# Kernel tuning notes

Measured on AMD Instinct MI355X. Metric: run time of the kernel, lower is better.

Reference implementation:

```python
import jax, jax.numpy as jnp
import numpy as np

HIDDEN = 2048
HEADS = 16
HEAD_DIM = HIDDEN // HEADS  # 128
ROPE_BASE = 10000.0


def _rope_cos_sin(seq_len, head_dim, dtype):
    inv_freq = 1.0 / (ROPE_BASE ** (jnp.arange(0, head_dim, 2, dtype=jnp.float32) / head_dim))
    pos = jnp.arange(seq_len, dtype=jnp.float32)
    freqs = pos[:, None] * inv_freq[None, :]            # [S, D/2]
    emb = jnp.concatenate([freqs, freqs], axis=-1)      # [S, D]
    return jnp.cos(emb).astype(dtype), jnp.sin(emb).astype(dtype)


def _rotate_half(x):
    x1, x2 = jnp.split(x, 2, axis=-1)
    return jnp.concatenate([-x2, x1], axis=-1)


def apply_rope(q, k, seq_len):
    # q, k: [B, H, S, Dh]
    cos, sin = _rope_cos_sin(seq_len, q.shape[-1], q.dtype)
    q = q * cos + _rotate_half(q) * sin
    k = k * cos + _rotate_half(k) * sin
    return q, k


def setup_inputs() -> dict:
    key = jax.random.key(0)
    ks = jax.random.split(key, 5)
    B, S = 2, 2048
    scale = 1.0 / np.sqrt(HIDDEN)
    return {
        "hidden_states": jax.random.normal(ks[0], (B, S, HIDDEN), dtype=jnp.float32),
        "w_qkv": jax.random.normal(ks[1], (3 * HIDDEN, HIDDEN), dtype=jnp.float32) * scale,
        "b_qkv": jnp.zeros((3 * HIDDEN,), dtype=jnp.float32),
        "w_dense": jax.random.normal(ks[2], (HIDDEN, HIDDEN), dtype=jnp.float32) * scale,
        "b_dense": jnp.zeros((HIDDEN,), dtype=jnp.float32),
    }


def reference(hidden_states, w_qkv, b_qkv, w_dense, b_dense):
    B, S, _ = hidden_states.shape
    qkv = hidden_states @ w_qkv.T + b_qkv                      # [B, S, 3*H*Dh]
    qkv = qkv.reshape(B, S, 3, HEADS, HEAD_DIM)
    qkv = jnp.transpose(qkv, (2, 0, 3, 1, 4))                  # [3, B, H, S, Dh]
    q, k, v = qkv[0], qkv[1], qkv[2]

    # pos_encoding.apply_to_qk -> RoPE
    q, k = apply_rope(q, k, S)

    scale = HEAD_DIM ** (-0.5)
    scores = jnp.einsum("bhqd,bhkd->bhqk", q, k) * scale       # [B, H, S, S]

    # pos_encoding.apply_to_scores -> causal additive mask
    causal = jnp.tril(jnp.ones((S, S), dtype=bool))
    scores = jnp.where(causal, scores, jnp.finfo(scores.dtype).min)

    attn = jax.nn.softmax(scores, axis=-1)
    out = jnp.einsum("bhqk,bhkd->bhqd", attn, v)               # [B, H, S, Dh]
    out = jnp.transpose(out, (0, 2, 1, 3)).reshape(B, S, HIDDEN)
    return out @ w_dense.T + b_dense
```

## Files before the change

kernel.cpp:

```cpp
#include <hip/hip_runtime.h>
#include <hip/hip_bf16.h>
#include <stdint.h>

#define HID 2048
#define NHEAD 16
#define DHEAD 128
#define BB 2
#define SS 2048
#define MM (BB*SS)
#define NQKV (3*HID)
#define NT (SS/64)

typedef __attribute__((ext_vector_type(8))) short bf16x8;
typedef __attribute__((ext_vector_type(4))) float f32x4;
typedef unsigned short ushort_t;

__device__ __forceinline__ f32x4 mfma16(bf16x8 a, bf16x8 b, f32x4 c) {
    return __builtin_amdgcn_mfma_f32_16x16x32_bf16(a, b, c, 0, 0, 0);
}

__device__ __forceinline__ float bf2f(ushort_t u) {
    unsigned int x = ((unsigned int)u) << 16;
    return __builtin_bit_cast(float, x);
}
__device__ __forceinline__ ushort_t f2bf(float f) {
    unsigned int x = __builtin_bit_cast(unsigned int, f);
    unsigned int r = (x + 0x7FFFu + ((x >> 16) & 1u)) >> 16;
    return (ushort_t)r;
}

__device__ __forceinline__ void cvt8(const float* __restrict__ g, ushort_t* l) {
    float4 a = *(const float4*)g;
    float4 b = *(const float4*)(g + 4);
    union { ushort_t u[8]; uint4 v; } t;
    t.u[0] = f2bf(a.x); t.u[1] = f2bf(a.y); t.u[2] = f2bf(a.z); t.u[3] = f2bf(a.w);
    t.u[4] = f2bf(b.x); t.u[5] = f2bf(b.y); t.u[6] = f2bf(b.z); t.u[7] = f2bf(b.w);
    *(uint4*)l = t.v;
}

__device__ __forceinline__ void gload16(const ushort_t* g, ushort_t* l) {
    __builtin_amdgcn_global_load_lds(
        (const __attribute__((address_space(1))) unsigned int*)(const void*)g,
        (__attribute__((address_space(3))) unsigned int*)(void*)l,
        16, 0, 0);
}

__global__ void cvt3_kernel(const float* __restrict__ a, ushort_t* __restrict__ da, int na,
                            const float* __restrict__ b, ushort_t* __restrict__ db, int nb,
                            const float* __restrict__ c, ushort_t* __restrict__ dc, int nc)
{
    int i = blockIdx.x * blockDim.x + threadIdx.x;
    if (i < na) {
        cvt8(a + (size_t)i * 8, da + (size_t)i * 8);
    } else if (i < na + nb) {
        int j = i - na;
        cvt8(b + (size_t)j * 8, db + (size_t)j * 8);
    } else if (i < na + nb + nc) {
        int j = i - na - nb;
        cvt8(c + (size_t)j * 8, dc + (size_t)j * 8);
    }
}

#define BM 256
#define BN 128
#define BKK 64
#define NTK (HID/BKK)
#define ASZ (BM*BKK)
#define BSZ (BN*BKK)
#define BUFSZ (ASZ+BSZ)

__global__ __launch_bounds__(512, 1) void qkv_gemm_fast(
    const ushort_t* __restrict__ X,
    const ushort_t* __restrict__ W,
    const float* __restrict__ bias,
    ushort_t* __restrict__ qws,
    ushort_t* __restrict__ kws,
    ushort_t* __restrict__ vtws)
{
    __shared__ __align__(16) ushort_t smem[3 * BUFSZ];

    const int tid  = threadIdx.x;
    const int lane = tid & 63;
    const int w    = tid >> 6;
    const int wm   = w >> 1;
    const int wn   = w & 1;
    const int quad = lane >> 4;
    const int l15  = lane & 15;
    const int sub  = (lane & 7) ^ (lane >> 3);
    const int rloc = lane >> 3;
    const int m0 = blockIdx.y * BM;
    const int n0 = blockIdx.x * BN;
    const bool vmode = (n0 >= 2 * HID);

    const ushort_t* gA = X + (size_t)m0 * HID;
    const ushort_t* gB = W + (size_t)n0 * HID;

    f32x4 acc[4][4];
#pragma unroll
    for (int i = 0; i < 4; i++)
#pragma unroll
        for (int j = 0; j < 4; j++)
#pragma unroll
            for (int e = 0; e < 4; e++) acc[i][j][e] = 0.f;

    auto STAGE = [&](int bufi, int t) {
        ushort_t* lA = smem + bufi * BUFSZ;
        ushort_t* lB = lA + ASZ;
        const ushort_t* ga = gA + t * BKK;
        const ushort_t* gb = gB + t * BKK;
#pragma unroll
        for (int i = 0; i < 4; i++) {
            int blk = w * 4 + i;
            gload16(ga + (size_t)(blk * 8 + rloc) * HID + sub * 8, lA + blk * 512);
        }
#pragma unroll
        for (int i = 0; i < 2; i++) {
            int blk = w * 2 + i;
            gload16(gb + (size_t)(blk * 8 + rloc) * HID + sub * 8, lB + blk * 512);
        }
    };

    auto COMPUTE = [&](int bufi) {
        const ushort_t* lA = smem + bufi * BUFSZ;
        const ushort_t* lB = lA + ASZ;
        bf16x8 af[2][4], bfr[2][4];
#pragma unroll
        for (int kk = 0; kk < 2; kk++) {
            const int cs = ((kk * 4 + quad) ^ (l15 & 7)) << 3;
#pragma unroll
            for (int mb = 0; mb < 4; mb++)
                af[kk][mb] = *(const bf16x8*)(lA + (wm * 64 + mb * 16 + l15) * 64 + cs);
#pragma unroll
            for (int nb = 0; nb < 4; nb++)
                bfr[kk][nb] = *(const bf16x8*)(lB + (wn * 64 + nb * 16 + l15) * 64 + cs);
        }
        __builtin_amdgcn_s_setprio(1);
        if (!vmode) {
#pragma unroll
            for (int kk = 0; kk < 2; kk++)
#pragma unroll
                for (int mb = 0; mb < 4; mb++)
#pragma unroll
                    for (int nb = 0; nb < 4; nb++)
                        acc[mb][nb] = mfma16(af[kk][mb], bfr[kk][nb], acc[mb][nb]);
        } else {
#pragma unroll
            for (int kk = 0; kk < 2; kk++)
#pragma unroll
                for (int mb = 0; mb < 4; mb++)
#pragma unroll
                    for (int nb = 0; nb < 4; nb++)
                        acc[mb][nb] = mfma16(bfr[kk][nb], af[kk][mb], acc[mb][nb]);
        }
        __builtin_amdgcn_s_setprio(0);
    };

    STAGE(0, 0);
    STAGE(1, 1);
    asm volatile("s_waitcnt vmcnt(6)" ::: "memory");
    __builtin_amdgcn_s_barrier();

    int buf = 0;
    for (int t = 0; t < NTK - 2; t++) {
        int b2 = buf + 2; if (b2 >= 3) b2 -= 3;
        STAGE(b2, t + 2);
        COMPUTE(buf);
        asm volatile("s_waitcnt vmcnt(6)" ::: "memory");
        __builtin_amdgcn_s_barrier();
        buf++; if (buf == 3) buf = 0;
    }
    COMPUTE(buf);
    asm volatile("s_waitcnt vmcnt(0)" ::: "memory");
    __builtin_amdgcn_s_barrier();
    buf++; if (buf == 3) buf = 0;
    COMPUTE(buf);

    if (!vmode) {
#pragma unroll
        for (int nb = 0; nb < 4; nb++) {
            int n = n0 + wn * 64 + nb * 16 + l15;
            float bv = bias[n];
            int mat = n >> 11;
            int h   = (n >> 7) & 15;
            int d   = n & 127;
            ushort_t* dst = (mat == 0) ? qws : kws;
#pragma unroll
            for (int mb = 0; mb < 4; mb++) {
#pragma unroll
                for (int r = 0; r < 4; r++) {
                    int m = m0 + wm * 64 + mb * 16 + quad * 4 + r;
                    int b = m >> 11;
                    int s = m & 2047;
                    dst[(((size_t)(b * 16 + h) * SS) + s) * DHEAD + d] =
                        f2bf(acc[mb][nb][r] + bv);
                }
            }
        }
    } else {
        const int b = m0 >> 11;
#pragma unroll
        for (int nb = 0; nb < 4; nb++) {
#pragma unroll
            for (int r = 0; r < 4; r++) {
                int n = n0 + wn * 64 + nb * 16 + quad * 4 + r;
                float bv = bias[n];
                int h = (n >> 7) & 15;
                int d = n & 127;
#pragma unroll
                for (int mb = 0; mb < 4; mb++) {
                    int s = (m0 & 2047) + wm * 64 + mb * 16 + l15;
                    vtws[(((size_t)(b * 16 + h) * DHEAD) + d) * SS + s] =
                        f2bf(acc[mb][nb][r] + bv);
                }
            }
        }
    }
}

__global__ __launch_bounds__(512, 1) void dense_gemm_fast(
    const ushort_t* __restrict__ A,
    const ushort_t* __restrict__ W,
    const float* __restrict__ bias,
    float* __restrict__ out)
{
    __shared__ __align__(16) ushort_t smem[3 * BUFSZ];

    const int tid  = threadIdx.x;
    const int lane = tid & 63;
    const int w    = tid >> 6;
    const int wm   = w >> 1;
    const int wn   = w & 1;
    const int quad = lane >> 4;
    const int l15  = lane & 15;
    const int sub  = (lane & 7) ^ (lane >> 3);
    const int rloc = lane >> 3;
    const int m0 = blockIdx.y * BM;
    const int n0 = blockIdx.x * BN;

    const ushort_t* gA = A + (size_t)m0 * HID;
    const ushort_t* gB = W + (size_t)n0 * HID;

    f32x4 acc[4][4];
#pragma unroll
    for (int i = 0; i < 4; i++)
#pragma unroll
        for (int j = 0; j < 4; j++)
#pragma unroll
            for (int e = 0; e < 4; e++) acc[i][j][e] = 0.f;

    auto STAGE = [&](int bufi, int t) {
        ushort_t* lA = smem + bufi * BUFSZ;
        ushort_t* lB = lA + ASZ;
        const ushort_t* ga = gA + t * BKK;
        const ushort_t* gb = gB + t * BKK;
#pragma unroll
        for (int i = 0; i < 4; i++) {
            int blk = w * 4 + i;
            gload16(ga + (size_t)(blk * 8 + rloc) * HID + sub * 8, lA + blk * 512);
        }
#pragma unroll
        for (int i = 0; i < 2; i++) {
            int blk = w * 2 + i;
            gload16(gb + (size_t)(blk * 8 + rloc) * HID + sub * 8, lB + blk * 512);
        }
    };

    auto COMPUTE = [&](int bufi) {
        const ushort_t* lA = smem + bufi * BUFSZ;
        const ushort_t* lB = lA + ASZ;
        bf16x8 af[2][4], bfr[2][4];
#pragma unroll
        for (int kk = 0; kk < 2; kk++) {
            const int cs = ((kk * 4 + quad) ^ (l15 & 7)) << 3;
#pragma unroll
            for (int mb = 0; mb < 4; mb++)
                af[kk][mb] = *(const bf16x8*)(lA + (wm * 64 + mb * 16 + l15) * 64 + cs);
#pragma unroll
            for (int nb = 0; nb < 4; nb++)
                bfr[kk][nb] = *(const bf16x8*)(lB + (wn * 64 + nb * 16 + l15) * 64 + cs);
        }
        __builtin_amdgcn_s_setprio(1);
#pragma unroll
        for (int kk = 0; kk < 2; kk++)
#pragma unroll
            for (int mb = 0; mb < 4; mb++)
#pragma unroll
                for (int nb = 0; nb < 4; nb++)
                    acc[mb][nb] = mfma16(af[kk][mb], bfr[kk][nb], acc[mb][nb]);
        __builtin_amdgcn_s_setprio(0);
    };

    STAGE(0, 0);
    STAGE(1, 1);
    asm volatile("s_waitcnt vmcnt(6)" ::: "memory");
    __builtin_amdgcn_s_barrier();

    int buf = 0;
    for (int t = 0; t < NTK - 2; t++) {
        int b2 = buf + 2; if (b2 >= 3) b2 -= 3;
        STAGE(b2, t + 2);
        COMPUTE(buf);
        asm volatile("s_waitcnt vmcnt(6)" ::: "memory");
        __builtin_amdgcn_s_barrier();
        buf++; if (buf == 3) buf = 0;
    }
    COMPUTE(buf);
    asm volatile("s_waitcnt vmcnt(0)" ::: "memory");
    __builtin_amdgcn_s_barrier();
    buf++; if (buf == 3) buf = 0;
    COMPUTE(buf);

#pragma unroll
    for (int nb = 0; nb < 4; nb++) {
        int n = n0 + wn * 64 + nb * 16 + l15;
        float bv = bias[n];
#pragma unroll
        for (int mb = 0; mb < 4; mb++) {
#pragma unroll
            for (int r = 0; r < 4; r++) {
                int m = m0 + wm * 64 + mb * 16 + quad * 4 + r;
                out[(size_t)m * HID + n] = acc[mb][nb][r] + bv;
            }
        }
    }
}

__global__ void rope_kernel2(ushort_t* __restrict__ qws, ushort_t* __restrict__ kws)
{
    int idx = blockIdx.x * blockDim.x + threadIdx.x;
    int d2 = idx & 63;
    int s  = idx >> 6;

    float inv_freq = exp2f(-(float)d2 * (13.287712379549449f / 64.f));
    float fr = (float)s * inv_freq;
    float sn, cs;
    sincosf(fr, &sn, &cs);

    size_t base0 = (size_t)s * DHEAD + d2;
#pragma unroll
    for (int bh = 0; bh < BB * NHEAD; bh++) {
        size_t base = base0 + (size_t)bh * (SS * DHEAD);
        float q1 = bf2f(qws[base]);
        float q2 = bf2f(qws[base + 64]);
        qws[base]      = f2bf(q1 * cs - q2 * sn);
        qws[base + 64] = f2bf(q2 * cs + q1 * sn);
        float k1 = bf2f(kws[base]);
        float k2 = bf2f(kws[base + 64]);
        kws[base]      = f2bf(k1 * cs - k2 * sn);
        kws[base + 64] = f2bf(k2 * cs + k1 * sn);
    }
}

#define LDP 72

__global__ __launch_bounds__(256, 2) void attn_kernel4(
    const ushort_t* __restrict__ qws,
    const ushort_t* __restrict__ kws,
    const ushort_t* __restrict__ vtws,
    ushort_t* __restrict__ aout)
{
    __shared__ __align__(16) ushort_t k_s[64 * 128];
    __shared__ __align__(16) ushort_t vt_s[128 * 64];
    __shared__ __align__(16) ushort_t pA_s[4][16 * LDP];
    __shared__ __align__(16) ushort_t pB_s[4][16 * LDP];

    const int tid  = threadIdx.x;
    const int lane = tid & 63;
    const int w    = tid >> 6;
    const int quad = lane >> 4;
    const int l15  = lane & 15;

    const int g  = blockIdx.x;
    const int bh = (g & 7) | (((g >> 3) & 3) << 3);
    const int tA = g >> 5;
    const int tB = NT - 1 - tA;
    const int qA = tA * 64, qB = tB * 64;
    const size_t qk_base = (size_t)bh * SS * DHEAD;

    bf16x8 qa[4], qb[4];
    {
        const ushort_t* rowA = qws + qk_base + (size_t)(qA + w * 16 + l15) * DHEAD;
        const ushort_t* rowB = qws + qk_base + (size_t)(qB + w * 16 + l15) * DHEAD;
#pragma unroll
        for (int kc = 0; kc < 4; kc++) {
            qa[kc] = *(const bf16x8*)(rowA + kc * 32 + quad * 8);
            qb[kc] = *(const bf16x8*)(rowB + kc * 32 + quad * 8);
        }
    }

    bf16x8 ones;
#pragma unroll
    for (int i = 0; i < 8; i++) ones[i] = (short)0x3F80;

    f32x4 oA[8], oB[8], lA, lB;
#pragma unroll
    for (int i = 0; i < 8; i++)
#pragma unroll
        for (int e = 0; e < 4; e++) { oA[i][e] = 0.f; oB[i][e] = 0.f; }
#pragma unroll
    for (int e = 0; e < 4; e++) { lA[e] = 0.f; lB[e] = 0.f; }

    const int srowK = lane >> 4;
    const int srowV = lane >> 3;
    const int ccgV  = (lane & 7) ^ (lane >> 3);

    const int q_baseA = qA + w * 16 + quad * 4;
    const int q_baseB = qB + w * 16 + quad * 4;
    const int xorv = l15 & 7;

    const float scale2 = 0.12753102015727466f;
    const float FM = 16.0f;

    for (int j = 0; j <= tB; j++) {
        const int kb = j * 64;
        __syncthreads();
#pragma unroll
        for (int i = 0; i < 4; i++) {
            int P = i * 4 + w;
            int row = P * 4 + srowK;
            int ccg = l15 ^ (((P & 1) * 4) + srowK);
            gload16(kws + qk_base + (size_t)(kb + row) * DHEAD + ccg * 8,
                    k_s + P * 512);
        }
#pragma unroll
        for (int i = 0; i < 4; i++) {
            int P = i * 4 + w;
            int row = P * 8 + srowV;
            gload16(vtws + qk_base + (size_t)row * SS + kb + ccgV * 8,
                    vt_s + P * 512);
        }
        __syncthreads();

        f32x4 sA[4], sB[4];
#pragma unroll
        for (int nb = 0; nb < 4; nb++)
#pragma unroll
            for (int e = 0; e < 4; e++) { sA[nb][e] = 0.f; sB[nb][e] = 0.f; }

        if (j <= tA) {
#pragma unroll
            for (int kc = 0; kc < 4; kc++) {
#pragma unroll
                for (int nb = 0; nb < 4; nb++) {
                    int cc_s = (kc * 4 + quad) ^ xorv;
                    bf16x8 kf = *(const bf16x8*)(k_s + (nb * 16 + l15) * 128 + cc_s * 8);
                    sA[nb] = mfma16(qa[kc], kf, sA[nb]);
                    sB[nb] = mfma16(qb[kc], kf, sB[nb]);
                }
            }
#pragma unroll
            for (int nb = 0; nb < 4; nb++) {
                int kidx = kb + nb * 16 + l15;
#pragma unroll
                for (int r = 0; r < 4; r++) {
                    float pa = exp2f(sA[nb][r] * scale2 - FM);
                    float pb = exp2f(sB[nb][r] * scale2 - FM);
                    pa = (kidx <= q_baseA + r) ? pa : 0.f;
                    pb = (kidx <= q_baseB + r) ? pb : 0.f;
                    pA_s[w][(quad * 4 + r) * LDP + nb * 16 + l15] = f2bf(pa);
                    pB_s[w][(quad * 4 + r) * LDP + nb * 16 + l15] = f2bf(pb);
                }
            }
#pragma unroll
            for (int kc = 0; kc < 2; kc++) {
                bf16x8 pa = *(const bf16x8*)(pA_s[w] + l15 * LDP + kc * 32 + quad * 8);
                bf16x8 pb = *(const bf16x8*)(pB_s[w] + l15 * LDP + kc * 32 + quad * 8);
                lA = mfma16(pa, ones, lA);
                lB = mfma16(pb, ones, lB);
#pragma unroll
                for (int db = 0; db < 8; db++) {
                    int cc_s = (kc * 4 + quad) ^ xorv;
                    bf16x8 vf = *(const bf16x8*)(vt_s + (db * 16 + l15) * 64 + cc_s * 8);
                    oA[db] = mfma16(pa, vf, oA[db]);
                    oB[db] = mfma16(pb, vf, oB[db]);
                }
            }
        } else {
#pragma unroll
            for (int kc = 0; kc < 4; kc++) {
#pragma unroll
                for (int nb = 0; nb < 4; nb++) {
                    int cc_s = (kc * 4 + quad) ^ xorv;
                    bf16x8 kf = *(const bf16x8*)(k_s + (nb * 16 + l15) * 128 + cc_s * 8);
                    sB[nb] = mfma16(qb[kc], kf, sB[nb]);
                }
            }
#pragma unroll
            for (int nb = 0; nb < 4; nb++) {
                int kidx = kb + nb * 16 + l15;
#pragma unroll
                for (int r = 0; r < 4; r++) {
                    float pb = exp2f(sB[nb][r] * scale2 - FM);
                    pb = (kidx <= q_baseB + r) ? pb : 0.f;
                    pB_s[w][(quad * 4 + r) * LDP + nb * 16 + l15] = f2bf(pb);
                }
            }
#pragma unroll
            for (int kc = 0; kc < 2; kc++) {
                bf16x8 pb = *(const bf16x8*)(pB_s[w] + l15 * LDP + kc * 32 + quad * 8);
                lB = mfma16(pb, ones, lB);
#pragma unroll
                for (int db = 0; db < 8; db++) {
                    int cc_s = (kc * 4 + quad) ^ xorv;
                    bf16x8 vf = *(const bf16x8*)(vt_s + (db * 16 + l15) * 64 + cc_s * 8);
                    oB[db] = mfma16(pb, vf, oB[db]);
                }
            }
        }
    }

    const int b = bh >> 4;
    const int h = bh & 15;
    float invA[4], invB[4];
#pragma unroll
    for (int r = 0; r < 4; r++) { invA[r] = 1.f / lA[r]; invB[r] = 1.f / lB[r]; }
#pragma unroll
    for (int db = 0; db < 8; db++) {
#pragma unroll
        for (int r = 0; r < 4; r++) {
            int sA_row = qA + w * 16 + quad * 4 + r;
            int sB_row = qB + w * 16 + quad * 4 + r;
            size_t offA = ((size_t)(b * SS + sA_row)) * HID + h * DHEAD + db * 16 + l15;
            size_t offB = ((size_t)(b * SS + sB_row)) * HID + h * DHEAD + db * 16 + l15;
            aout[offA] = f2bf(oA[db][r] * invA[r]);
            aout[offB] = f2bf(oB[db][r] * invB[r]);
        }
    }
}

extern "C" void kernel_launch(void* const* d_in, const int* in_sizes, int n_in,
                              void* d_out, int out_size, void* d_ws, size_t ws_size,
                              hipStream_t stream)
{
    const float* X    = (const float*)d_in[0];
    const float* Wqkv = (const float*)d_in[1];
    const float* bqkv = (const float*)d_in[2];
    const float* Wd   = (const float*)d_in[3];
    const float* bd   = (const float*)d_in[4];
    float* out = (float*)d_out;

    char* ws = (char*)d_ws;
    const size_t MB = 1048576;
    ushort_t* qws  = (ushort_t*)(ws);
    ushort_t* kws  = (ushort_t*)(ws + 16 * MB);
    ushort_t* vtws = (ushort_t*)(ws + 32 * MB);
    ushort_t* aout = (ushort_t*)(ws + 48 * MB);
    ushort_t* Xbf  = (ushort_t*)(ws + 48 * MB);
    ushort_t* Wqbf = (ushort_t*)(ws + 64 * MB);
    ushort_t* Wdbf = (ushort_t*)(ws + 88 * MB);

    const int nX = MM * HID / 8, nWq = NQKV * HID / 8, nWd = HID * HID / 8;
    cvt3_kernel<<<(nX + nWq + nWd + 255) / 256, 256, 0, stream>>>(
        X, Xbf, nX, Wqkv, Wqbf, nWq, Wd, Wdbf, nWd);

    qkv_gemm_fast<<<dim3(NQKV / BN, MM / BM), 512, 0, stream>>>(Xbf, Wqbf, bqkv, qws, kws, vtws);
    rope_kernel2<<<(SS * 64) / 256, 256, 0, stream>>>(qws, kws);
    attn_kernel4<<<dim3(NT / 2 * BB * NHEAD), 256, 0, stream>>>(qws, kws, vtws, aout);
    dense_gemm_fast<<<dim3(HID / BN, MM / BM), 512, 0, stream>>>(aout, Wdbf, bd, out);
}
```

Before: 376.2 us.

## Replace QKV GEMM with 256x256 eight-phase pipelined kernel and vectorize RoPE

The QKV projection moves to a new 256x256-tile GEMM with a double-buffered LDS slot. Each k-step is split into four quarter-tile phases that interleave global-to-LDS loads of the next tile with MFMA work on the current one. The goal is better operand reuse and latency hiding than the 256x128 triple-buffer kernel. The RoPE kernel is also rewritten so each thread handles 8 contiguous dims with 16-byte loads and stores over 4 heads. This cuts scalar 2-byte memory traffic, but each thread now does more sincos work per element. The larger accumulator tile raises register pressure, and the many barriers add synchronization cost.

```diff
diff --git a/kernel.cpp b/kernel.cpp
--- a/kernel.cpp
+++ b/kernel.cpp
@@ -44,6 +44,11 @@
         (__attribute__((address_space(3))) unsigned int*)(void*)l,
         16, 0, 0);
 }
+
+#define WAITV0 asm volatile("s_waitcnt vmcnt(0)" ::: "memory")
+#define WAITV2 asm volatile("s_waitcnt vmcnt(2)" ::: "memory")
+#define WAITV4 asm volatile("s_waitcnt vmcnt(4)" ::: "memory")
+#define BAR()  __builtin_amdgcn_s_barrier()
 
 __global__ void cvt3_kernel(const float* __restrict__ a, ushort_t* __restrict__ da, int na,
                             const float* __restrict__ b, ushort_t* __restrict__ db, int nb,
@@ -61,6 +66,204 @@
     }
 }
 
+#define QBM 256
+#define QBN 256
+#define QBK 64
+#define QNT (HID/QBK)
+#define QTSZ (256*64)
+#define QSLOT (2*QTSZ)
+
+__global__ __launch_bounds__(512, 2) void qkv_gemm_8ph(
+    const ushort_t* __restrict__ X,
+    const ushort_t* __restrict__ W,
+    const float* __restrict__ bias,
+    ushort_t* __restrict__ qws,
+    ushort_t* __restrict__ kws,
+    ushort_t* __restrict__ vtws)
+{
+    __shared__ __align__(16) ushort_t smem[2 * QSLOT];
+
+    const int tid  = threadIdx.x;
+    const int lane = tid & 63;
+    const int w    = tid >> 6;
+    const int wm   = w >> 2;
+    const int wn   = w & 3;
+    const int quad = lane >> 4;
+    const int l15  = lane & 15;
+    const int sub  = (lane & 7) ^ (lane >> 3);
+    const int rloc = lane >> 3;
+    const int m0 = blockIdx.y * QBM;
+    const int n0 = blockIdx.x * QBN;
+    const bool vmode = (n0 >= 2 * HID);
+
+    const ushort_t* gA = X + (size_t)m0 * HID;
+    const ushort_t* gB = W + (size_t)n0 * HID;
+
+    f32x4 acc[8][4];
+#pragma unroll
+    for (int i = 0; i < 8; i++)
+#pragma unroll
+        for (int j = 0; j < 4; j++)
+#pragma unroll
+            for (int e = 0; e < 4; e++) acc[i][j][e] = 0.f;
+
+    auto SHA = [&](int slot, int t, int h) {
+        ushort_t* l = smem + slot * QSLOT;
+#pragma unroll
+        for (int r = 0; r < 2; r++) {
+            int rowb = r * 128 + h * 64 + w * 8;
+            gload16(gA + (size_t)(rowb + rloc) * HID + t * QBK + sub * 8,
+                    l + rowb * 64);
+        }
+    };
+    auto SHB = [&](int slot, int t, int h) {
+        ushort_t* l = smem + slot * QSLOT + QTSZ;
+#pragma unroll
+        for (int r = 0; r < 2; r++) {
+            int idx  = r * 64 + w * 8;
+            int rowb = ((idx >> 5) << 6) + h * 32 + (idx & 31);
+            gload16(gB + (size_t)(rowb + rloc) * HID + t * QBK + sub * 8,
+                    l + rowb * 64);
+        }
+    };
+
+    bf16x8 aCur[2][4], bEv[2][2], bOd[2][2];
+
+    auto READ_A = [&](int slot, int mh) {
+        const ushort_t* lA = smem + slot * QSLOT;
+#pragma unroll
+        for (int kk = 0; kk < 2; kk++) {
+            const int csw = ((kk * 4 + quad) ^ (l15 & 7)) * 8;
+#pragma unroll
+            for (int i = 0; i < 4; i++)
+                aCur[kk][i] = *(const bf16x8*)(lA + (wm * 128 + mh * 64 + i * 16 + l15) * 64 + csw);
+        }
+    };
+    auto READ_B = [&](int slot, int nh, bf16x8 (*b)[2]) {
+        const ushort_t* lB = smem + slot * QSLOT + QTSZ;
+#pragma unroll
+        for (int kk = 0; kk < 2; kk++) {
+            const int csw = ((kk * 4 + quad) ^ (l15 & 7)) * 8;
+#pragma unroll
+            for (int j = 0; j < 2; j++)
+                b[kk][j] = *(const bf16x8*)(lB + (wn * 64 + nh * 32 + j * 16 + l15) * 64 + csw);
+        }
+    };
+    auto MFMA_Q = [&](int mh, int nh, bf16x8 (*b)[2]) {
+        __builtin_amdgcn_s_setprio(1);
+        if (!vmode) {
+#pragma unroll
+            for (int kk = 0; kk < 2; kk++)
+#pragma unroll
+                for (int i = 0; i < 4; i++)
+#pragma unroll
+                    for (int j = 0; j < 2; j++)
+                        acc[mh*4+i][nh*2+j] = mfma16(aCur[kk][i], b[kk][j], acc[mh*4+i][nh*2+j]);
+        } else {
+#pragma unroll
+            for (int kk = 0; kk < 2; kk++)
+#pragma unroll
+                for (int i = 0; i < 4; i++)
+#pragma unroll
+                    for (int j = 0; j < 2; j++)
+                        acc[mh*4+i][nh*2+j] = mfma16(b[kk][j], aCur[kk][i], acc[mh*4+i][nh*2+j]);
+        }
+        __builtin_amdgcn_s_setprio(0);
+    };
+
+    SHA(0, 0, 0);
+    SHB(0, 0, 0);
+    SHB(0, 0, 1);
+    SHA(0, 0, 1);
+    WAITV4;
+    BAR();
+
+    for (int t = 0; t < QNT - 1; t++) {
+        const int c = t & 1, n = c ^ 1;
+        SHA(n, t + 1, 0);
+        READ_A(c, 0); READ_B(c, 0, bEv);
+        WAITV4;
+        BAR();
+        MFMA_Q(0, 0, bEv);
+        BAR();
+        SHB(n, t + 1, 0);
+        READ_B(c, 1, bOd);
+        WAITV4;
+        BAR();
+        MFMA_Q(0, 1, bOd);
+        BAR();
+        SHB(n, t + 1, 1);
+        READ_A(c, 1);
+        BAR();
+        MFMA_Q(1, 1, bOd);
+        BAR();
+        SHA(n, t + 1, 1);
+        WAITV4;
+        BAR();
+        MFMA_Q(1, 0, bEv);
+        BAR();
+    }
+    {
+        const int c = (QNT - 1) & 1;
+        READ_A(c, 0); READ_B(c, 0, bEv);
+        WAITV2;
+        BAR();
+        MFMA_Q(0, 0, bEv);
+        BAR();
+        READ_B(c, 1, bOd);
+        WAITV0;
+        BAR();
+        MFMA_Q(0, 1, bOd);
+        BAR();
+        READ_A(c, 1);
+        BAR();
+        MFMA_Q(1, 1, bOd);
+        BAR();
+        MFMA_Q(1, 0, bEv);
+    }
+
+    if (!vmode) {
+#pragma unroll
+        for (int nj = 0; nj < 4; nj++) {
+            int n = n0 + wn * 64 + nj * 16 + l15;
+            float bv = bias[n];
+            int mat = n >> 11;
+            int h   = (n >> 7) & 15;
+            int d   = n & 127;
+            ushort_t* dst = (mat == 0) ? qws : kws;
+#pragma unroll
+            for (int mi = 0; mi < 8; mi++) {
+#pragma unroll
+                for (int r = 0; r < 4; r++) {
+                    int m = m0 + wm * 128 + mi * 16 + quad * 4 + r;
+                    int b = m >> 11;
+                    int s = m & 2047;
+                    dst[(((size_t)(b * 16 + h) * SS) + s) * DHEAD + d] =
+                        f2bf(acc[mi][nj][r] + bv);
+                }
+            }
+        }
+    } else {
+        const int b = m0 >> 11;
+#pragma unroll
+        for (int nj = 0; nj < 4; nj++) {
+#pragma unroll
+            for (int r = 0; r < 4; r++) {
+                int n = n0 + wn * 64 + nj * 16 + quad * 4 + r;
+                float bv = bias[n];
+                int h = (n >> 7) & 15;
+                int d = n & 127;
+#pragma unroll
+                for (int mi = 0; mi < 8; mi++) {
+                    int s = (m0 & 2047) + wm * 128 + mi * 16 + l15;
+                    vtws[(((size_t)(b * 16 + h) * DHEAD) + d) * SS + s] =
+                        f2bf(acc[mi][nj][r] + bv);
+                }
+            }
+        }
+    }
+}
+
 #define BM 256
 #define BN 128
 #define BKK 64
@@ -69,13 +272,11 @@
 #define BSZ (BN*BKK)
 #define BUFSZ (ASZ+BSZ)
 
-__global__ __launch_bounds__(512, 1) void qkv_gemm_fast(
-    const ushort_t* __restrict__ X,
+__global__ __launch_bounds__(512, 1) void dense_gemm_fast(
+    const ushort_t* __restrict__ A,
     const ushort_t* __restrict__ W,
     const float* __restrict__ bias,
-    ushort_t* __restrict__ qws,
-    ushort_t* __restrict__ kws,
-    ushort_t* __restrict__ vtws)
+    float* __restrict__ out)
 {
     __shared__ __align__(16) ushort_t smem[3 * BUFSZ];
 
@@ -90,9 +291,8 @@
     const int rloc = lane >> 3;
     const int m0 = blockIdx.y * BM;
     const int n0 = blockIdx.x * BN;
-    const bool vmode = (n0 >= 2 * HID);
-
-    const ushort_t* gA = X + (size_t)m0 * HID;
+
+    const ushort_t* gA = A + (size_t)m0 * HID;
     const ushort_t* gB = W + (size_t)n0 * HID;
 
     f32x4 acc[4][4];
@@ -135,23 +335,13 @@
                 bfr[kk][nb] = *(const bf16x8*)(lB + (wn * 64 + nb * 16 + l15) * 64 + cs);
         }
         __builtin_amdgcn_s_setprio(1);
-        if (!vmode) {
-#pragma unroll
-            for (int kk = 0; kk < 2; kk++)
-#pragma unroll
-                for (int mb = 0; mb < 4; mb++)
-#pragma unroll
-                    for (int nb = 0; nb < 4; nb++)
-                        acc[mb][nb] = mfma16(af[kk][mb], bfr[kk][nb], acc[mb][nb]);
-        } else {
-#pragma unroll
-            for (int kk = 0; kk < 2; kk++)
-#pragma unroll
-                for (int mb = 0; mb < 4; mb++)
-#pragma unroll
-                    for (int nb = 0; nb < 4; nb++)
-                        acc[mb][nb] = mfma16(bfr[kk][nb], af[kk][mb], acc[mb][nb]);
-        }
+#pragma unroll
+        for (int kk = 0; kk < 2; kk++)
+#pragma unroll
+            for (int mb = 0; mb < 4; mb++)
+#pragma unroll
+                for (int nb = 0; nb < 4; nb++)
+                    acc[mb][nb] = mfma16(af[kk][mb], bfr[kk][nb], acc[mb][nb]);
         __builtin_amdgcn_s_setprio(0);
     };
 
@@ -175,141 +365,6 @@
     buf++; if (buf == 3) buf = 0;
     COMPUTE(buf);
 
-    if (!vmode) {
-#pragma unroll
-        for (int nb = 0; nb < 4; nb++) {
-            int n = n0 + wn * 64 + nb * 16 + l15;
-            float bv = bias[n];
-            int mat = n >> 11;
-            int h   = (n >> 7) & 15;
-            int d   = n & 127;
-            ushort_t* dst = (mat == 0) ? qws : kws;
-#pragma unroll
-            for (int mb = 0; mb < 4; mb++) {
-#pragma unroll
-                for (int r = 0; r < 4; r++) {
-                    int m = m0 + wm * 64 + mb * 16 + quad * 4 + r;
-                    int b = m >> 11;
-                    int s = m & 2047;
-                    dst[(((size_t)(b * 16 + h) * SS) + s) * DHEAD + d] =
-                        f2bf(acc[mb][nb][r] + bv);
-                }
-            }
-        }
-    } else {
-        const int b = m0 >> 11;
-#pragma unroll
-        for (int nb = 0; nb < 4; nb++) {
-#pragma unroll
-            for (int r = 0; r < 4; r++) {
-                int n = n0 + wn * 64 + nb * 16 + quad * 4 + r;
-                float bv = bias[n];
-                int h = (n >> 7) & 15;
-                int d = n & 127;
-#pragma unroll
-                for (int mb = 0; mb < 4; mb++) {
-                    int s = (m0 & 2047) + wm * 64 + mb * 16 + l15;
-                    vtws[(((size_t)(b * 16 + h) * DHEAD) + d) * SS + s] =
-                        f2bf(acc[mb][nb][r] + bv);
-                }
-            }
-        }
-    }
-}
-
-__global__ __launch_bounds__(512, 1) void dense_gemm_fast(
-    const ushort_t* __restrict__ A,
-    const ushort_t* __restrict__ W,
-    const float* __restrict__ bias,
-    float* __restrict__ out)
-{
-    __shared__ __align__(16) ushort_t smem[3 * BUFSZ];
-
-    const int tid  = threadIdx.x;
-    const int lane = tid & 63;
-    const int w    = tid >> 6;
-    const int wm   = w >> 1;
-    const int wn   = w & 1;
-    const int quad = lane >> 4;
-    const int l15  = lane & 15;
-    const int sub  = (lane & 7) ^ (lane >> 3);
-    const int rloc = lane >> 3;
-    const int m0 = blockIdx.y * BM;
-    const int n0 = blockIdx.x * BN;
-
-    const ushort_t* gA = A + (size_t)m0 * HID;
-    const ushort_t* gB = W + (size_t)n0 * HID;
-
-    f32x4 acc[4][4];
-#pragma unroll
-    for (int i = 0; i < 4; i++)
-#pragma unroll
-        for (int j = 0; j < 4; j++)
-#pragma unroll
-            for (int e = 0; e < 4; e++) acc[i][j][e] = 0.f;
-
-    auto STAGE = [&](int bufi, int t) {
-        ushort_t* lA = smem + bufi * BUFSZ;
-        ushort_t* lB = lA + ASZ;
-        const ushort_t* ga = gA + t * BKK;
-        const ushort_t* gb = gB + t * BKK;
-#pragma unroll
-        for (int i = 0; i < 4; i++) {
-            int blk = w * 4 + i;
-            gload16(ga + (size_t)(blk * 8 + rloc) * HID + sub * 8, lA + blk * 512);
-        }
-#pragma unroll
-        for (int i = 0; i < 2; i++) {
-            int blk = w * 2 + i;
-            gload16(gb + (size_t)(blk * 8 + rloc) * HID + sub * 8, lB + blk * 512);
-        }
-    };
-
-    auto COMPUTE = [&](int bufi) {
-        const ushort_t* lA = smem + bufi * BUFSZ;
-        const ushort_t* lB = lA + ASZ;
-        bf16x8 af[2][4], bfr[2][4];
-#pragma unroll
-        for (int kk = 0; kk < 2; kk++) {
-            const int cs = ((kk * 4 + quad) ^ (l15 & 7)) << 3;
-#pragma unroll
-            for (int mb = 0; mb < 4; mb++)
-                af[kk][mb] = *(const bf16x8*)(lA + (wm * 64 + mb * 16 + l15) * 64 + cs);
-#pragma unroll
-            for (int nb = 0; nb < 4; nb++)
-                bfr[kk][nb] = *(const bf16x8*)(lB + (wn * 64 + nb * 16 + l15) * 64 + cs);
-        }
-        __builtin_amdgcn_s_setprio(1);
-#pragma unroll
-        for (int kk = 0; kk < 2; kk++)
-#pragma unroll
-            for (int mb = 0; mb < 4; mb++)
-#pragma unroll
-                for (int nb = 0; nb < 4; nb++)
-                    acc[mb][nb] = mfma16(af[kk][mb], bfr[kk][nb], acc[mb][nb]);
-        __builtin_amdgcn_s_setprio(0);
-    };
-
-    STAGE(0, 0);
-    STAGE(1, 1);
-    asm volatile("s_waitcnt vmcnt(6)" ::: "memory");
-    __builtin_amdgcn_s_barrier();
-
-    int buf = 0;
-    for (int t = 0; t < NTK - 2; t++) {
-        int b2 = buf + 2; if (b2 >= 3) b2 -= 3;
-        STAGE(b2, t + 2);
-        COMPUTE(buf);
-        asm volatile("s_waitcnt vmcnt(6)" ::: "memory");
-        __builtin_amdgcn_s_barrier();
-        buf++; if (buf == 3) buf = 0;
-    }
-    COMPUTE(buf);
-    asm volatile("s_waitcnt vmcnt(0)" ::: "memory");
-    __builtin_amdgcn_s_barrier();
-    buf++; if (buf == 3) buf = 0;
-    COMPUTE(buf);
-
 #pragma unroll
     for (int nb = 0; nb < 4; nb++) {
         int n = n0 + wn * 64 + nb * 16 + l15;
@@ -325,29 +380,52 @@
     }
 }
 
-__global__ void rope_kernel2(ushort_t* __restrict__ qws, ushort_t* __restrict__ kws)
+__global__ void rope_kernel3(ushort_t* __restrict__ qws, ushort_t* __restrict__ kws)
 {
-    int idx = blockIdx.x * blockDim.x + threadIdx.x;
-    int d2 = idx & 63;
-    int s  = idx >> 6;
-
-    float inv_freq = exp2f(-(float)d2 * (13.287712379549449f / 64.f));
-    float fr = (float)s * inv_freq;
-    float sn, cs;
-    sincosf(fr, &sn, &cs);
-
-    size_t base0 = (size_t)s * DHEAD + d2;
-#pragma unroll
-    for (int bh = 0; bh < BB * NHEAD; bh++) {
-        size_t base = base0 + (size_t)bh * (SS * DHEAD);
-        float q1 = bf2f(qws[base]);
-        float q2 = bf2f(qws[base + 64]);
-        qws[base]      = f2bf(q1 * cs - q2 * sn);
-        qws[base + 64] = f2bf(q2 * cs + q1 * sn);
-        float k1 = bf2f(kws[base]);
-        float k2 = bf2f(kws[base + 64]);
-        kws[base]      = f2bf(k1 * cs - k2 * sn);
-        kws[base + 64] = f2bf(k2 * cs + k1 * sn);
+    int t = blockIdx.x * blockDim.x + threadIdx.x;
+    int d2g = t & 7;
+    int s   = (t >> 3) & 2047;
+    int bh0 = (t >> 14) * 4;
+
+    float sn[8], cs[8];
+#pragma unroll
+    for (int jj = 0; jj < 8; jj++) {
+        int d2 = d2g * 8 + jj;
+        float inv_freq = exp2f(-(float)d2 * (13.287712379549449f / 64.f));
+        float fr = (float)s * inv_freq;
+        sincosf(fr, &sn[jj], &cs[jj]);
+    }
+
+    size_t base0 = (size_t)s * DHEAD + d2g * 8;
+#pragma unroll
+    for (int q = 0; q < 4; q++) {
+        size_t base = base0 + (size_t)(bh0 + q) * (SS * DHEAD);
+        {
+            union { ushort_t u[8]; uint4 v; } x1, x2, y1, y2;
+            x1.v = *(const uint4*)(qws + base);
+            x2.v = *(const uint4*)(qws + base + 64);
+#pragma unroll
+            for (int jj = 0; jj < 8; jj++) {
+                float a = bf2f(x1.u[jj]), b = bf2f(x2.u[jj]);
+                y1.u[jj] = f2bf(a * cs[jj] - b * sn[jj]);
+                y2.u[jj] = f2bf(b * cs[jj] + a * sn[jj]);
+            }
+            *(uint4*)(qws + base) = y1.v;
+            *(uint4*)(qws + base + 64) = y2.v;
+        }
+        {
+            union { ushort_t u[8]; uint4 v; } x1, x2, y1, y2;
+            x1.v = *(const uint4*)(kws + base);
+            x2.v = *(const uint4*)(kws + base + 64);
+#pragma unroll
+            for (int jj = 0; jj < 8; jj++) {
+                float a = bf2f(x1.u[jj]), b = bf2f(x2.u[jj]);
+                y1.u[jj] = f2bf(a * cs[jj] - b * sn[jj]);
+                y2.u[jj] = f2bf(b * cs[jj] + a * sn[jj]);
+            }
+            *(uint4*)(kws + base) = y1.v;
+            *(uint4*)(kws + base + 64) = y2.v;
+        }
     }
 }
 
@@ -553,8 +631,8 @@
     cvt3_kernel<<<(nX + nWq + nWd + 255) / 256, 256, 0, stream>>>(
         X, Xbf, nX, Wqkv, Wqbf, nWq, Wd, Wdbf, nWd);
 
-    qkv_gemm_fast<<<dim3(NQKV / BN, MM / BM), 512, 0, stream>>>(Xbf, Wqbf, bqkv, qws, kws, vtws);
-    rope_kernel2<<<(SS * 64) / 256, 256, 0, stream>>>(qws, kws);
+    qkv_gemm_8ph<<<dim3(NQKV / QBN, MM / QBM), 512, 0, stream>>>(Xbf, Wqbf, bqkv, qws, kws, vtws);
+    rope_kernel3<<<(SS * 8 * 8) / 256, 256, 0, stream>>>(qws, kws);
     attn_kernel4<<<dim3(NT / 2 * BB * NHEAD), 256, 0, stream>>>(qws, kws, vtws, aout);
     dense_gemm_fast<<<dim3(HID / BN, MM / BM), 512, 0, stream>>>(aout, Wdbf, bd, out);
 }
```

New measurement: 459.5 us. +22.1%, slower.

## Double-buffer K tiles in attention and vectorize the RoPE kernel

Applied to the files above, without the earlier changes.

The attention kernel now double-buffers its K tile in shared memory, prefetching the next K block and loading V asynchronously during the score computation, with split vmcnt waits so the QK^T MFMAs overlap the global loads. The RoPE kernel is rewritten to process 8 contiguous dims per thread with 16-byte vector loads and stores over 4 heads, replacing scalar bf16 accesses. The trade-offs are more LDS use per block, which may lower occupancy, extra barriers per iteration, and repeated sincos evaluation per thread group.

```diff
diff --git a/kernel.cpp b/kernel.cpp
--- a/kernel.cpp
+++ b/kernel.cpp
@@ -44,6 +44,12 @@
         (__attribute__((address_space(3))) unsigned int*)(void*)l,
         16, 0, 0);
 }
+
+#define WAITV0 asm volatile("s_waitcnt vmcnt(0)" ::: "memory")
+#define WAITV4 asm volatile("s_waitcnt vmcnt(4)" ::: "memory")
+#define WAITV6 asm volatile("s_waitcnt vmcnt(6)" ::: "memory")
+#define WAITV8 asm volatile("s_waitcnt vmcnt(8)" ::: "memory")
+#define BAR()  __builtin_amdgcn_s_barrier()
 
 __global__ void cvt3_kernel(const float* __restrict__ a, ushort_t* __restrict__ da, int na,
                             const float* __restrict__ b, ushort_t* __restrict__ db, int nb,
@@ -82,8 +88,7 @@
     const int tid  = threadIdx.x;
     const int lane = tid & 63;
     const int w    = tid >> 6;
-    const int wm   = w >> 1;
-    const int wn   = w & 1;
+    const int wm   = w >> 1, wn = w & 1;
     const int quad = lane >> 4;
     const int l15  = lane & 15;
     const int sub  = (lane & 7) ^ (lane >> 3);
@@ -157,21 +162,21 @@
 
     STAGE(0, 0);
     STAGE(1, 1);
-    asm volatile("s_waitcnt vmcnt(6)" ::: "memory");
-    __builtin_amdgcn_s_barrier();
+    WAITV6;
+    BAR();
 
     int buf = 0;
     for (int t = 0; t < NTK - 2; t++) {
         int b2 = buf + 2; if (b2 >= 3) b2 -= 3;
         STAGE(b2, t + 2);
         COMPUTE(buf);
-        asm volatile("s_waitcnt vmcnt(6)" ::: "memory");
-        __builtin_amdgcn_s_barrier();
+        WAITV6;
+        BAR();
         buf++; if (buf == 3) buf = 0;
     }
     COMPUTE(buf);
-    asm volatile("s_waitcnt vmcnt(0)" ::: "memory");
-    __builtin_amdgcn_s_barrier();
+    WAITV0;
+    BAR();
     buf++; if (buf == 3) buf = 0;
     COMPUTE(buf);
 
@@ -292,21 +297,21 @@
 
     STAGE(0, 0);
     STAGE(1, 1);
-    asm volatile("s_waitcnt vmcnt(6)" ::: "memory");
-    __builtin_amdgcn_s_barrier();
+    WAITV6;
+    BAR();
 
     int buf = 0;
     for (int t = 0; t < NTK - 2; t++) {
         int b2 = buf + 2; if (b2 >= 3) b2 -= 3;
         STAGE(b2, t + 2);
         COMPUTE(buf);
-        asm volatile("s_waitcnt vmcnt(6)" ::: "memory");
-        __builtin_amdgcn_s_barrier();
+        WAITV6;
+        BAR();
         buf++; if (buf == 3) buf = 0;
     }
     COMPUTE(buf);
-    asm volatile("s_waitcnt vmcnt(0)" ::: "memory");
-    __builtin_amdgcn_s_barrier();
+    WAITV0;
+    BAR();
     buf++; if (buf == 3) buf = 0;
     COMPUTE(buf);
 
@@ -325,41 +330,64 @@
     }
 }
 
-__global__ void rope_kernel2(ushort_t* __restrict__ qws, ushort_t* __restrict__ kws)
+__global__ void rope_kernel3(ushort_t* __restrict__ qws, ushort_t* __restrict__ kws)
 {
-    int idx = blockIdx.x * blockDim.x + threadIdx.x;
-    int d2 = idx & 63;
-    int s  = idx >> 6;
-
-    float inv_freq = exp2f(-(float)d2 * (13.287712379549449f / 64.f));
-    float fr = (float)s * inv_freq;
-    float sn, cs;
-    sincosf(fr, &sn, &cs);
-
-    size_t base0 = (size_t)s * DHEAD + d2;
-#pragma unroll
-    for (int bh = 0; bh < BB * NHEAD; bh++) {
-        size_t base = base0 + (size_t)bh * (SS * DHEAD);
-        float q1 = bf2f(qws[base]);
-        float q2 = bf2f(qws[base + 64]);
-        qws[base]      = f2bf(q1 * cs - q2 * sn);
-        qws[base + 64] = f2bf(q2 * cs + q1 * sn);
-        float k1 = bf2f(kws[base]);
-        float k2 = bf2f(kws[base + 64]);
-        kws[base]      = f2bf(k1 * cs - k2 * sn);
-        kws[base + 64] = f2bf(k2 * cs + k1 * sn);
+    int t = blockIdx.x * blockDim.x + threadIdx.x;
+    int d2g = t & 7;
+    int s   = (t >> 3) & 2047;
+    int bh0 = (t >> 14) * 4;
+
+    float sn[8], cs[8];
+#pragma unroll
+    for (int jj = 0; jj < 8; jj++) {
+        int d2 = d2g * 8 + jj;
+        float inv_freq = exp2f(-(float)d2 * (13.287712379549449f / 64.f));
+        float fr = (float)s * inv_freq;
+        sincosf(fr, &sn[jj], &cs[jj]);
+    }
+
+    size_t base0 = (size_t)s * DHEAD + d2g * 8;
+#pragma unroll
+    for (int q = 0; q < 4; q++) {
+        size_t base = base0 + (size_t)(bh0 + q) * (SS * DHEAD);
+        {
+            union { ushort_t u[8]; uint4 v; } x1, x2, y1, y2;
+            x1.v = *(const uint4*)(qws + base);
+            x2.v = *(const uint4*)(qws + base + 64);
+#pragma unroll
+            for (int jj = 0; jj < 8; jj++) {
+                float a = bf2f(x1.u[jj]), b = bf2f(x2.u[jj]);
+                y1.u[jj] = f2bf(a * cs[jj] - b * sn[jj]);
+                y2.u[jj] = f2bf(b * cs[jj] + a * sn[jj]);
+            }
+            *(uint4*)(qws + base) = y1.v;
+            *(uint4*)(qws + base + 64) = y2.v;
+        }
+        {
+            union { ushort_t u[8]; uint4 v; } x1, x2, y1, y2;
+            x1.v = *(const uint4*)(kws + base);
+            x2.v = *(const uint4*)(kws + base + 64);
+#pragma unroll
+            for (int jj = 0; jj < 8; jj++) {
+                float a = bf2f(x1.u[jj]), b = bf2f(x2.u[jj]);
+                y1.u[jj] = f2bf(a * cs[jj] - b * sn[jj]);
+                y2.u[jj] = f2bf(b * cs[jj] + a * sn[jj]);
+            }
+            *(uint4*)(kws + base) = y1.v;
+            *(uint4*)(kws + base + 64) = y2.v;
+        }
     }
 }
 
 #define LDP 72
 
-__global__ __launch_bounds__(256, 2) void attn_kernel4(
+__global__ __launch_bounds__(256, 2) void attn_kernel5(
     const ushort_t* __restrict__ qws,
     const ushort_t* __restrict__ kws,
     const ushort_t* __restrict__ vtws,
     ushort_t* __restrict__ aout)
 {
-    __shared__ __align__(16) ushort_t k_s[64 * 128];
+    __shared__ __align__(16) ushort_t k_s[2][64 * 128];
     __shared__ __align__(16) ushort_t vt_s[128 * 64];
     __shared__ __align__(16) ushort_t pA_s[4][16 * LDP];
     __shared__ __align__(16) ushort_t pB_s[4][16 * LDP];
@@ -411,17 +439,19 @@
     const float scale2 = 0.12753102015727466f;
     const float FM = 16.0f;
 
-    for (int j = 0; j <= tB; j++) {
+    auto KSTAGE = [&](int j, int slot) {
         const int kb = j * 64;
-        __syncthreads();
 #pragma unroll
         for (int i = 0; i < 4; i++) {
             int P = i * 4 + w;
             int row = P * 4 + srowK;
             int ccg = l15 ^ (((P & 1) * 4) + srowK);
             gload16(kws + qk_base + (size_t)(kb + row) * DHEAD + ccg * 8,
-                    k_s + P * 512);
-        }
+                    k_s[slot] + P * 512);
+        }
+    };
+    auto VSTAGE = [&](int j) {
+        const int kb = j * 64;
 #pragma unroll
         for (int i = 0; i < 4; i++) {
             int P = i * 4 + w;
@@ -429,13 +459,30 @@
             gload16(vtws + qk_base + (size_t)row * SS + kb + ccgV * 8,
                     vt_s + P * 512);
         }
-        __syncthreads();
+    };
+
+    KSTAGE(0, 0);
+
+    for (int j = 0; j <= tB; j++) {
+        const int kb = j * 64;
+        const int slot = j & 1;
+
+        VSTAGE(j);
+        if (j < tB) {
+            KSTAGE(j + 1, slot ^ 1);
+            WAITV8;
+        } else {
+            WAITV4;
+        }
+        BAR();
 
         f32x4 sA[4], sB[4];
 #pragma unroll
         for (int nb = 0; nb < 4; nb++)
 #pragma unroll
             for (int e = 0; e < 4; e++) { sA[nb][e] = 0.f; sB[nb][e] = 0.f; }
+
+        const ushort_t* ks = k_s[slot];
 
         if (j <= tA) {
 #pragma unroll
@@ -443,7 +490,7 @@
 #pragma unroll
                 for (int nb = 0; nb < 4; nb++) {
                     int cc_s = (kc * 4 + quad) ^ xorv;
-                    bf16x8 kf = *(const bf16x8*)(k_s + (nb * 16 + l15) * 128 + cc_s * 8);
+                    bf16x8 kf = *(const bf16x8*)(ks + (nb * 16 + l15) * 128 + cc_s * 8);
                     sA[nb] = mfma16(qa[kc], kf, sA[nb]);
                     sB[nb] = mfma16(qb[kc], kf, sB[nb]);
                 }
@@ -461,6 +508,8 @@
                     pB_s[w][(quad * 4 + r) * LDP + nb * 16 + l15] = f2bf(pb);
                 }
             }
+            if (j < tB) { WAITV4; } else { WAITV0; }
+            BAR();
 #pragma unroll
             for (int kc = 0; kc < 2; kc++) {
                 bf16x8 pa = *(const bf16x8*)(pA_s[w] + l15 * LDP + kc * 32 + quad * 8);
@@ -481,7 +530,7 @@
 #pragma unroll
                 for (int nb = 0; nb < 4; nb++) {
                     int cc_s = (kc * 4 + quad) ^ xorv;
-                    bf16x8 kf = *(const bf16x8*)(k_s + (nb * 16 + l15) * 128 + cc_s * 8);
+                    bf16x8 kf = *(const bf16x8*)(ks + (nb * 16 + l15) * 128 + cc_s * 8);
                     sB[nb] = mfma16(qb[kc], kf, sB[nb]);
                 }
             }
@@ -495,6 +544,8 @@
                     pB_s[w][(quad * 4 + r) * LDP + nb * 16 + l15] = f2bf(pb);
                 }
             }
+            if (j < tB) { WAITV4; } else { WAITV0; }
+            BAR();
 #pragma unroll
             for (int kc = 0; kc < 2; kc++) {
                 bf16x8 pb = *(const bf16x8*)(pB_s[w] + l15 * LDP + kc * 32 + quad * 8);
@@ -507,6 +558,7 @@
                 }
             }
         }
+        BAR();
     }
 
     const int b = bh >> 4;
@@ -554,7 +606,7 @@
         X, Xbf, nX, Wqkv, Wqbf, nWq, Wd, Wdbf, nWd);
 
     qkv_gemm_fast<<<dim3(NQKV / BN, MM / BM), 512, 0, stream>>>(Xbf, Wqbf, bqkv, qws, kws, vtws);
-    rope_kernel2<<<(SS * 64) / 256, 256, 0, stream>>>(qws, kws);
-    attn_kernel4<<<dim3(NT / 2 * BB * NHEAD), 256, 0, stream>>>(qws, kws, vtws, aout);
+    rope_kernel3<<<(SS * 8 * 8) / 256, 256, 0, stream>>>(qws, kws);
+    attn_kernel5<<<dim3(NT / 2 * BB * NHEAD), 256, 0, stream>>>(qws, kws, vtws, aout);
     dense_gemm_fast<<<dim3(HID / BN, MM / BM), 512, 0, stream>>>(aout, Wdbf, bd, out);
 }
```

New measurement: 375.3 us. About the same (-0.2%).
